# Kernel optimization log

Measured on AMD Instinct MI355X. Metric: run time of the kernel, lower is better.

Reference implementation:

```python
import jax, jax.numpy as jnp
import numpy as np

VOCAB, EMB, LAYERS, OUT, N = 32000, 43, 64, 15, 524288

def setup_inputs() -> dict:
    key = jax.random.key(0)
    ks = jax.random.split(key, 8)
    emb = jax.random.normal(ks[0], (VOCAB, EMB), jnp.float32) * 0.1
    emb = emb.at[0].set(0.0)  # padding_idx=0
    return {
        "tokens": jax.random.randint(ks[1], (N,), 0, VOCAB, jnp.int32),
        "emb": emb,
        "w_ih": jax.random.normal(ks[2], (LAYERS, 4 * EMB, EMB), jnp.float32) * 0.1,
        "w_hh": jax.random.normal(ks[3], (LAYERS, 4 * EMB, EMB), jnp.float32) * 0.1,
        "b_ih": jax.random.normal(ks[4], (LAYERS, 4 * EMB), jnp.float32) * 0.1,
        "b_hh": jax.random.normal(ks[5], (LAYERS, 4 * EMB), jnp.float32) * 0.1,
        "w_out": jax.random.normal(ks[6], (OUT, EMB), jnp.float32) * 0.1,
        "b_out": jax.random.normal(ks[7], (OUT,), jnp.float32) * 0.1,
    }

def reference(tokens, emb, w_ih, w_hh, b_ih, b_hh, w_out, b_out):
    # embedding lookup; dropout is identity in eval mode
    x = emb[tokens]  # (N, EMB)

    # 64-layer LSTM stack, seq_len=1, h0=c0=0 => f-gate * c_prev and W_hh @ h_prev vanish,
    # but we implement the full PyTorch LSTM cell math (gate order i, f, g, o).
    def layer(h, params):
        wi, wh, bi, bh = params
        h_prev = jnp.zeros_like(h)  # initial hidden state per layer
        gates = h @ wi.T + bi + h_prev @ wh.T + bh  # (N, 4*EMB)
        i, f, g, o = jnp.split(gates, 4, axis=-1)
        c = jax.nn.sigmoid(f) * 0.0 + jax.nn.sigmoid(i) * jnp.tanh(g)
        h_new = jax.nn.sigmoid(o) * jnp.tanh(c)
        return h_new, None

    h, _ = jax.lax.scan(layer, x, (w_ih, w_hh, b_ih, b_hh))
    logits = h @ w_out.T + b_out  # (N, OUT)
    return jax.nn.log_softmax(logits, axis=1)
```

## Files before the change

### kernel.cpp

```cpp
#include <hip/hip_runtime.h>

#define LAYERS 64
#define EMBD   43
#define NOUT   15
#define NTOK   524288

#define ROWB     128
#define WROWS    144
#define IMGBYTES (WROWS * ROWB)
#define NCHUNK   18

#define MBLK    256
#define THREADS 256

#define NEG_L2E   -1.44269504f
#define NEG_2L2E  -2.88539008f

typedef short bf16x8 __attribute__((ext_vector_type(8)));
typedef float f32x4  __attribute__((ext_vector_type(4)));
typedef float f32x2  __attribute__((ext_vector_type(2)));

__device__ __forceinline__ unsigned short f2bf(float f) {
  unsigned int u = __builtin_bit_cast(unsigned int, f);
  u = u + 0x7fffu + ((u >> 16) & 1u);
  return (unsigned short)(u >> 16);
}
__device__ __forceinline__ float bf2f(unsigned short s) {
  unsigned int u = ((unsigned int)s) << 16;
  return __builtin_bit_cast(float, u);
}

__global__ void pack_w_kernel(const float* __restrict__ w_ih,
                              const float* __restrict__ b_ih,
                              const float* __restrict__ b_hh,
                              unsigned char* __restrict__ wpack) {
  int idx = blockIdx.x * blockDim.x + threadIdx.x;
  if (idx >= LAYERS * WROWS) return;
  int l = idx / WROWS, n = idx % WROWS;
  int t = n >> 4, c = n & 15;
  int G = t / 3, gidx = t % 3;
  int gsel = (gidx == 0) ? 0 : ((gidx == 1) ? 2 : 3);
  float scale = (gidx == 1) ? NEG_2L2E : NEG_L2E;
  int j = (G == 0) ? 2 * c : ((G == 1) ? 2 * c + 1 : 32 + c);
  int valid = (j < EMBD);
  const float* src = w_ih + ((size_t)l * 172 + (size_t)gsel * EMBD + j) * EMBD;
  float bias = 0.0f;
  if (valid) {
    int R = gsel * EMBD + j;
    bias = (b_ih[l * 172 + R] + b_hh[l * 172 + R]) * scale;
  }
  unsigned char* dst = wpack + (size_t)l * IMGBYTES + n * ROWB;
  #pragma unroll
  for (int g = 0; g < 8; ++g) {
    union { unsigned short s[8]; uint4 v; } pk;
    #pragma unroll
    for (int e = 0; e < 8; ++e) {
      int k = g * 8 + e;
      unsigned short val = 0;
      if (valid && k < EMBD) val = f2bf(src[k] * scale);
      else if (valid && k == EMBD) val = f2bf(bias);
      pk.s[e] = val;
    }
    int slot = g ^ (n & 7);
    *(uint4*)(dst + slot * 16) = pk.v;
  }
}

__global__ void __launch_bounds__(THREADS, 3) lstm_kernel(
    const int* __restrict__ tokens,
    const float* __restrict__ emb,
    const unsigned char* __restrict__ wpack,
    const float* __restrict__ w_out,
    const float* __restrict__ b_out,
    float* __restrict__ out) {
  __shared__ __align__(16) unsigned char Hs[MBLK * ROWB];
  __shared__ __align__(16) unsigned char Ws[IMGBYTES];

  const int tid  = threadIdx.x;
  const int lane = tid & 63;
  const int wave = tid >> 6;
  const int c    = lane & 15;
  const int q    = lane >> 4;
  const int row_base = blockIdx.x * MBLK;

  {
    const unsigned char* src = wpack;
    #pragma unroll
    for (int ch = 0; ch < 5; ++ch) {
      int chunk = wave + ch * 4;
      if (chunk < NCHUNK)
        __builtin_amdgcn_global_load_lds(
            (const __attribute__((address_space(1))) void*)(src + chunk * 1024 + lane * 16),
            (__attribute__((address_space(3))) void*)(Ws + chunk * 1024),
            16, 0, 0);
    }
  }

  {
    int r = tid;
    int tok = tokens[row_base + r];
    const float* e = emb + (size_t)tok * EMBD;
    unsigned short v[64];
    #pragma unroll
    for (int k = 0; k < EMBD; ++k) v[k] = f2bf(e[k]);
    v[EMBD] = 0x3F80;
    #pragma unroll
    for (int k = EMBD + 1; k < 64; ++k) v[k] = 0;
    #pragma unroll
    for (int g = 0; g < 8; ++g) {
      union { unsigned short s[8]; uint4 u; } pk;
      #pragma unroll
      for (int e2 = 0; e2 < 8; ++e2) pk.s[e2] = v[g * 8 + e2];
      *(uint4*)(Hs + r * ROWB + ((g ^ (r & 7)) * 16)) = pk.u;
    }
  }

  int adrA0, adrA1, adrB0, adrB1, adrP[4], adrS[4];
  {
    int ra = wave * 64 + c;
    adrA0 = ra * ROWB + ((q ^ (c & 7)) * 16);
    adrA1 = ra * ROWB + (((4 + q) ^ (c & 7)) * 16);
    adrB0 = c * ROWB + ((q ^ (c & 7)) * 16);
    adrB1 = c * ROWB + (((4 + q) ^ (c & 7)) * 16);
    #pragma unroll
    for (int r4 = 0; r4 < 4; ++r4) {
      int rq = q * 4 + r4;
      int rm = rq & 7;
      int rr = wave * 64 + rq;
      adrP[r4] = rr * ROWB + (((c >> 2) ^ rm) * 16) + (c & 3) * 4;
      adrS[r4] = rr * ROWB + (((4 + (c >> 3)) ^ rm) * 16) + (c & 7) * 2;
    }
  }
  __syncthreads();

  const f32x4 zf = {0.0f, 0.0f, 0.0f, 0.0f};

  #pragma unroll 1
  for (int l = 0; l < LAYERS; ++l) {
    bf16x8 A0[4], A1[4];
    #pragma unroll
    for (int st = 0; st < 4; ++st) {
      A0[st] = *(const bf16x8*)(Hs + adrA0 + st * 2048);
      A1[st] = *(const bf16x8*)(Hs + adrA1 + st * 2048);
    }

    float hh[16];

    #pragma unroll
    for (int G = 0; G < 3; ++G) {
      f32x4 acc[3][4];
      #pragma unroll
      for (int t2 = 0; t2 < 3; ++t2) {
        int off = (G * 3 + t2) * 2048;
        bf16x8 B0 = *(const bf16x8*)(Ws + adrB0 + off);
        #pragma unroll
        for (int st = 0; st < 4; ++st)
          acc[t2][st] = __builtin_amdgcn_mfma_f32_16x16x32_bf16(A0[st], B0, zf, 0, 0, 0);
      }
      #pragma unroll
      for (int t2 = 0; t2 < 3; ++t2) {
        int off = (G * 3 + t2) * 2048;
        bf16x8 B1 = *(const bf16x8*)(Ws + adrB1 + off);
        #pragma unroll
        for (int st = 0; st < 4; ++st)
          acc[t2][st] = __builtin_amdgcn_mfma_f32_16x16x32_bf16(A1[st], B1, acc[t2][st], 0, 0, 0);
      }

      if (G == 2) {
        __syncthreads();
        if (l + 1 < LAYERS) {
          const unsigned char* src = wpack + (size_t)(l + 1) * IMGBYTES;
          #pragma unroll
          for (int ch = 0; ch < 5; ++ch) {
            int chunk = wave + ch * 4;
            if (chunk < NCHUNK)
              __builtin_amdgcn_global_load_lds(
                  (const __attribute__((address_space(1))) void*)(src + chunk * 1024 + lane * 16),
                  (__attribute__((address_space(3))) void*)(Ws + chunk * 1024),
                  16, 0, 0);
          }
        }
      }

      #pragma unroll
      for (int st = 0; st < 4; ++st) {
        #pragma unroll
        for (int hp = 0; hp < 2; ++hp) {
          const int r0 = hp * 2, r1 = hp * 2 + 1;
          f32x2 t1, t2v, t3;
          t1[0]  = __builtin_amdgcn_exp2f(acc[0][st][r0]);
          t1[1]  = __builtin_amdgcn_exp2f(acc[0][st][r1]);
          t2v[0] = __builtin_amdgcn_exp2f(acc[1][st][r0]);
          t2v[1] = __builtin_amdgcn_exp2f(acc[1][st][r1]);
          t3[0]  = __builtin_amdgcn_exp2f(acc[2][st][r0]);
          t3[1]  = __builtin_amdgcn_exp2f(acc[2][st][r1]);
          const f32x2 one = {1.0f, 1.0f};
          const f32x2 two = {2.0f, 2.0f};
          const f32x2 k15 = {15.0f, 15.0f};
          const f32x2 k25 = {2.5f, 2.5f};
          const f32x2 k6  = {6.0f, 6.0f};
          f32x2 u   = t2v + one;
          f32x2 Qd  = __builtin_elementwise_fma(t1, u, u);
          f32x2 P   = two - u;
          f32x2 x   = P * P;
          f32x2 y   = Qd * Qd;
          f32x2 n1  = __builtin_elementwise_fma(y, k15, x);
          f32x2 dt  = __builtin_elementwise_fma(y, k25, x);
          f32x2 nP  = P * n1;
          f32x2 dQ  = Qd * dt;
          f32x2 v6  = __builtin_elementwise_fma(t3, k6, k6);
          f32x2 den = dQ * v6;
          float h0 = nP[0] * __builtin_amdgcn_rcpf(den[0]);
          float h1 = nP[1] * __builtin_amdgcn_rcpf(den[1]);
          if (G == 0) {
            hh[st * 4 + r0] = h0;
            hh[st * 4 + r1] = h1;
          } else if (G == 1) {
            {
              unsigned int u0 = __builtin_bit_cast(unsigned int, hh[st * 4 + r0]) + 0x8000u;
              unsigned int u1 = __builtin_bit_cast(unsigned int, h0) + 0x8000u;
              unsigned int pk = __builtin_amdgcn_perm(u1, u0, 0x07060302u);
              *(unsigned int*)(Hs + adrP[r0] + st * 2048) = pk;
            }
            {
              unsigned int u0 = __builtin_bit_cast(unsigned int, hh[st * 4 + r1]) + 0x8000u;
              unsigned int u1 = __builtin_bit_cast(unsigned int, h1) + 0x8000u;
              unsigned int pk = __builtin_amdgcn_perm(u1, u0, 0x07060302u);
              *(unsigned int*)(Hs + adrP[r1] + st * 2048) = pk;
            }
          } else if (c <= 10) {
            unsigned int u1 = (__builtin_bit_cast(unsigned int, h0) + 0x8000u) >> 16;
            *(unsigned short*)(Hs + adrS[r0] + st * 2048) = (unsigned short)u1;
            unsigned int u2 = (__builtin_bit_cast(unsigned int, h1) + 0x8000u) >> 16;
            *(unsigned short*)(Hs + adrS[r1] + st * 2048) = (unsigned short)u2;
          }
        }
      }
    }
    __syncthreads();
  }

  {
    int r = tid;
    float h[EMBD];
    #pragma unroll
    for (int g = 0; g < 6; ++g) {
      union { uint4 u; unsigned short s[8]; } pk;
      pk.u = *(const uint4*)(Hs + r * ROWB + ((g ^ (r & 7)) * 16));
      #pragma unroll
      for (int e2 = 0; e2 < 8; ++e2) {
        int k = g * 8 + e2;
        if (k < EMBD) h[k] = bf2f(pk.s[e2]);
      }
    }
    float logit[NOUT];
    #pragma unroll
    for (int o = 0; o < NOUT; ++o) {
      float sum = b_out[o];
      #pragma unroll
      for (int k = 0; k < EMBD; ++k) sum += w_out[o * EMBD + k] * h[k];
      logit[o] = sum;
    }
    float m = logit[0];
    #pragma unroll
    for (int o = 1; o < NOUT; ++o) m = fmaxf(m, logit[o]);
    float ss = 0.0f;
    #pragma unroll
    for (int o = 0; o < NOUT; ++o) ss += __expf(logit[o] - m);
    float lse = m + __logf(ss);
    float* dst = out + (size_t)(row_base + r) * NOUT;
    #pragma unroll
    for (int o = 0; o < NOUT; ++o) dst[o] = logit[o] - lse;
  }
}

extern "C" void kernel_launch(void* const* d_in, const int* in_sizes, int n_in,
                              void* d_out, int out_size, void* d_ws, size_t ws_size,
                              hipStream_t stream) {
  const int* tokens     = (const int*)d_in[0];
  const float* emb      = (const float*)d_in[1];
  const float* w_ih     = (const float*)d_in[2];
  const float* b_ih     = (const float*)d_in[4];
  const float* b_hh     = (const float*)d_in[5];
  const float* w_out    = (const float*)d_in[6];
  const float* b_out    = (const float*)d_in[7];
  float* out            = (float*)d_out;

  const size_t need = (size_t)LAYERS * IMGBYTES;
  unsigned char* wpack = (ws_size >= need) ? (unsigned char*)d_ws
                                           : (unsigned char*)d_in[3];

  pack_w_kernel<<<(LAYERS * WROWS + 255) / 256, 256, 0, stream>>>(w_ih, b_ih, b_hh, wpack);
  lstm_kernel<<<NTOK / MBLK, THREADS, 0, stream>>>(tokens, emb, wpack, w_out, b_out, out);
}
```

Baseline: 1.058 ms.

## Shrink LDS row stride to 96 bytes to fit four blocks per CU

Cuts the padded K dimension from 64 to 48 bf16 per row for both the hidden-state tile and the weight image, using a new swizzle for the shorter rows. Lanes in the upper half of the second K step read from a small zeroed LDS region instead of real data. Total LDS per block drops from about 50KB to about 38KB, and launch bounds are raised from 3 to 4 blocks per CU to get more occupancy. In exchange the addressing is more complex, bank conflicts may rise, and there is more register pressure under the tighter bound.

Measured after the change: 1.082 ms. 1.02x slower.

```diff
diff --git a/kernel.cpp b/kernel.cpp
--- a/kernel.cpp
+++ b/kernel.cpp
@@ -5,13 +5,18 @@
 #define NOUT   15
 #define NTOK   524288
 
-#define ROWB     128
-#define WROWS    144
-#define IMGBYTES (WROWS * ROWB)
-#define NCHUNK   18
-
 #define MBLK    256
 #define THREADS 256
+
+#define ROWB      96
+#define WROWS     144
+#define IMGBYTES  (WROWS * ROWB)
+#define IMGSTRIDE 14336
+#define NCHUNK    14
+
+#define HSBYTES   (MBLK * ROWB)
+#define ZOFF      (HSBYTES + IMGSTRIDE)
+#define SBYTES    (ZOFF + 16)
 
 #define NEG_L2E   -1.44269504f
 #define NEG_2L2E  -2.88539008f
@@ -28,6 +33,11 @@
 __device__ __forceinline__ float bf2f(unsigned short s) {
   unsigned int u = ((unsigned int)s) << 16;
   return __builtin_bit_cast(float, u);
+}
+
+__device__ __forceinline__ int slotbyte(int g, int row) {
+  return (g < 4) ? (((g + (row >> 2)) & 3) * 16)
+                 : (64 + (((g - 4) ^ ((row >> 2) & 1)) * 16));
 }
 
 __global__ void pack_w_kernel(const float* __restrict__ w_ih,
@@ -49,9 +59,9 @@
     int R = gsel * EMBD + j;
     bias = (b_ih[l * 172 + R] + b_hh[l * 172 + R]) * scale;
   }
-  unsigned char* dst = wpack + (size_t)l * IMGBYTES + n * ROWB;
+  unsigned char* dst = wpack + (size_t)l * IMGSTRIDE + n * ROWB;
   #pragma unroll
-  for (int g = 0; g < 8; ++g) {
+  for (int g = 0; g < 6; ++g) {
     union { unsigned short s[8]; uint4 v; } pk;
     #pragma unroll
     for (int e = 0; e < 8; ++e) {
@@ -61,20 +71,18 @@
       else if (valid && k == EMBD) val = f2bf(bias);
       pk.s[e] = val;
     }
-    int slot = g ^ (n & 7);
-    *(uint4*)(dst + slot * 16) = pk.v;
-  }
-}
-
-__global__ void __launch_bounds__(THREADS, 3) lstm_kernel(
+    *(uint4*)(dst + slotbyte(g, n)) = pk.v;
+  }
+}
+
+__global__ void __launch_bounds__(THREADS, 4) lstm_kernel(
     const int* __restrict__ tokens,
     const float* __restrict__ emb,
     const unsigned char* __restrict__ wpack,
     const float* __restrict__ w_out,
     const float* __restrict__ b_out,
     float* __restrict__ out) {
-  __shared__ __align__(16) unsigned char Hs[MBLK * ROWB];
-  __shared__ __align__(16) unsigned char Ws[IMGBYTES];
+  __shared__ __align__(16) unsigned char S[SBYTES];
 
   const int tid  = threadIdx.x;
   const int lane = tid & 63;
@@ -86,12 +94,12 @@
   {
     const unsigned char* src = wpack;
     #pragma unroll
-    for (int ch = 0; ch < 5; ++ch) {
+    for (int ch = 0; ch < 4; ++ch) {
       int chunk = wave + ch * 4;
       if (chunk < NCHUNK)
         __builtin_amdgcn_global_load_lds(
             (const __attribute__((address_space(1))) void*)(src + chunk * 1024 + lane * 16),
-            (__attribute__((address_space(3))) void*)(Ws + chunk * 1024),
+            (__attribute__((address_space(3))) void*)(S + HSBYTES + chunk * 1024),
             16, 0, 0);
     }
   }
@@ -100,35 +108,44 @@
     int r = tid;
     int tok = tokens[row_base + r];
     const float* e = emb + (size_t)tok * EMBD;
-    unsigned short v[64];
+    unsigned short v[48];
     #pragma unroll
     for (int k = 0; k < EMBD; ++k) v[k] = f2bf(e[k]);
     v[EMBD] = 0x3F80;
     #pragma unroll
-    for (int k = EMBD + 1; k < 64; ++k) v[k] = 0;
-    #pragma unroll
-    for (int g = 0; g < 8; ++g) {
+    for (int k = EMBD + 1; k < 48; ++k) v[k] = 0;
+    #pragma unroll
+    for (int g = 0; g < 6; ++g) {
       union { unsigned short s[8]; uint4 u; } pk;
       #pragma unroll
       for (int e2 = 0; e2 < 8; ++e2) pk.s[e2] = v[g * 8 + e2];
-      *(uint4*)(Hs + r * ROWB + ((g ^ (r & 7)) * 16)) = pk.u;
-    }
-  }
-
-  int adrA0, adrA1, adrB0, adrB1, adrP[4], adrS[4];
+      *(uint4*)(S + r * ROWB + slotbyte(g, r)) = pk.u;
+    }
+    if (tid == 0) {
+      uint4 z4 = {0u, 0u, 0u, 0u};
+      *(uint4*)(S + ZOFF) = z4;
+    }
+  }
+
+  int adrA0, adrA1, adrB0, adrB1, incHi, adrP[4], adrSg[4];
   {
     int ra = wave * 64 + c;
-    adrA0 = ra * ROWB + ((q ^ (c & 7)) * 16);
-    adrA1 = ra * ROWB + (((4 + q) ^ (c & 7)) * 16);
-    adrB0 = c * ROWB + ((q ^ (c & 7)) * 16);
-    adrB1 = c * ROWB + (((4 + q) ^ (c & 7)) * 16);
+    adrA0 = ra * ROWB + (((q + (c >> 2)) & 3) * 16);
+    adrB0 = HSBYTES + c * ROWB + (((q + (c >> 2)) & 3) * 16);
+    if (q < 2) {
+      adrA1 = ra * ROWB + 64 + ((q ^ ((c >> 2) & 1)) * 16);
+      adrB1 = HSBYTES + c * ROWB + 64 + ((q ^ ((c >> 2) & 1)) * 16);
+      incHi = 16 * ROWB;
+    } else {
+      adrA1 = ZOFF;
+      adrB1 = ZOFF;
+      incHi = 0;
+    }
     #pragma unroll
     for (int r4 = 0; r4 < 4; ++r4) {
-      int rq = q * 4 + r4;
-      int rm = rq & 7;
-      int rr = wave * 64 + rq;
-      adrP[r4] = rr * ROWB + (((c >> 2) ^ rm) * 16) + (c & 3) * 4;
-      adrS[r4] = rr * ROWB + (((4 + (c >> 3)) ^ rm) * 16) + (c & 7) * 2;
+      int rr = wave * 64 + q * 4 + r4;
+      adrP[r4]  = rr * ROWB + ((((c >> 2) + q) & 3) * 16) + (c & 3) * 4;
+      adrSg[r4] = rr * ROWB + 64 + (((c >> 3) ^ (q & 1)) * 16) + (c & 7) * 2;
     }
   }
   __syncthreads();
@@ -138,29 +155,34 @@
   #pragma unroll 1
   for (int l = 0; l < LAYERS; ++l) {
     bf16x8 A0[4], A1[4];
-    #pragma unroll
-    for (int st = 0; st < 4; ++st) {
-      A0[st] = *(const bf16x8*)(Hs + adrA0 + st * 2048);
-      A1[st] = *(const bf16x8*)(Hs + adrA1 + st * 2048);
+    {
+      int a1 = adrA1;
+      #pragma unroll
+      for (int st = 0; st < 4; ++st) {
+        A0[st] = *(const bf16x8*)(S + adrA0 + st * (16 * ROWB));
+        A1[st] = *(const bf16x8*)(S + a1);
+        a1 += incHi;
+      }
     }
 
     float hh[16];
+    int b1 = adrB1;
 
     #pragma unroll
     for (int G = 0; G < 3; ++G) {
       f32x4 acc[3][4];
       #pragma unroll
       for (int t2 = 0; t2 < 3; ++t2) {
-        int off = (G * 3 + t2) * 2048;
-        bf16x8 B0 = *(const bf16x8*)(Ws + adrB0 + off);
+        int off = (G * 3 + t2) * (16 * ROWB);
+        bf16x8 B0 = *(const bf16x8*)(S + adrB0 + off);
         #pragma unroll
         for (int st = 0; st < 4; ++st)
           acc[t2][st] = __builtin_amdgcn_mfma_f32_16x16x32_bf16(A0[st], B0, zf, 0, 0, 0);
       }
       #pragma unroll
       for (int t2 = 0; t2 < 3; ++t2) {
-        int off = (G * 3 + t2) * 2048;
-        bf16x8 B1 = *(const bf16x8*)(Ws + adrB1 + off);
+        bf16x8 B1 = *(const bf16x8*)(S + b1);
+        b1 += incHi;
         #pragma unroll
         for (int st = 0; st < 4; ++st)
           acc[t2][st] = __builtin_amdgcn_mfma_f32_16x16x32_bf16(A1[st], B1, acc[t2][st], 0, 0, 0);
@@ -169,14 +191,14 @@
       if (G == 2) {
         __syncthreads();
         if (l + 1 < LAYERS) {
-          const unsigned char* src = wpack + (size_t)(l + 1) * IMGBYTES;
+          const unsigned char* src = wpack + (size_t)(l + 1) * IMGSTRIDE;
           #pragma unroll
-          for (int ch = 0; ch < 5; ++ch) {
+          for (int ch = 0; ch < 4; ++ch) {
             int chunk = wave + ch * 4;
             if (chunk < NCHUNK)
               __builtin_amdgcn_global_load_lds(
                   (const __attribute__((address_space(1))) void*)(src + chunk * 1024 + lane * 16),
-                  (__attribute__((address_space(3))) void*)(Ws + chunk * 1024),
+                  (__attribute__((address_space(3))) void*)(S + HSBYTES + chunk * 1024),
                   16, 0, 0);
           }
         }
@@ -220,19 +242,19 @@
               unsigned int u0 = __builtin_bit_cast(unsigned int, hh[st * 4 + r0]) + 0x8000u;
               unsigned int u1 = __builtin_bit_cast(unsigned int, h0) + 0x8000u;
               unsigned int pk = __builtin_amdgcn_perm(u1, u0, 0x07060302u);
-              *(unsigned int*)(Hs + adrP[r0] + st * 2048) = pk;
+              *(unsigned int*)(S + adrP[r0] + st * (16 * ROWB)) = pk;
             }
             {
               unsigned int u0 = __builtin_bit_cast(unsigned int, hh[st * 4 + r1]) + 0x8000u;
               unsigned int u1 = __builtin_bit_cast(unsigned int, h1) + 0x8000u;
               unsigned int pk = __builtin_amdgcn_perm(u1, u0, 0x07060302u);
-              *(unsigned int*)(Hs + adrP[r1] + st * 2048) = pk;
+              *(unsigned int*)(S + adrP[r1] + st * (16 * ROWB)) = pk;
             }
           } else if (c <= 10) {
             unsigned int u1 = (__builtin_bit_cast(unsigned int, h0) + 0x8000u) >> 16;
-            *(unsigned short*)(Hs + adrS[r0] + st * 2048) = (unsigned short)u1;
+            *(unsigned short*)(S + adrSg[r0] + st * (16 * ROWB)) = (unsigned short)u1;
             unsigned int u2 = (__builtin_bit_cast(unsigned int, h1) + 0x8000u) >> 16;
-            *(unsigned short*)(Hs + adrS[r1] + st * 2048) = (unsigned short)u2;
+            *(unsigned short*)(S + adrSg[r1] + st * (16 * ROWB)) = (unsigned short)u2;
           }
         }
       }
@@ -246,7 +268,7 @@
     #pragma unroll
     for (int g = 0; g < 6; ++g) {
       union { uint4 u; unsigned short s[8]; } pk;
-      pk.u = *(const uint4*)(Hs + r * ROWB + ((g ^ (r & 7)) * 16));
+      pk.u = *(const uint4*)(S + r * ROWB + slotbyte(g, r));
       #pragma unroll
       for (int e2 = 0; e2 < 8; ++e2) {
         int k = g * 8 + e2;
@@ -286,7 +308,7 @@
   const float* b_out    = (const float*)d_in[7];
   float* out            = (float*)d_out;
 
-  const size_t need = (size_t)LAYERS * IMGBYTES;
+  const size_t need = (size_t)LAYERS * IMGSTRIDE;
   unsigned char* wpack = (ws_size >= need) ? (unsigned char*)d_ws
                                            : (unsigned char*)d_in[3];
 
```

## Load per-lane packed LSTM weight fragments from global, dropping LDS staging and block barriers

Applied to the files above, without the earlier changes.

The weight packer now writes each layer in an MFMA B-fragment order, so every lane can fetch its bf16x8 fragment directly from global memory with coalesced 16-byte loads. This removes the shared-memory weight image, the per-layer async global-to-LDS copies and both per-layer __syncthreads. It relies on each wave reading and writing only its own hidden-state rows. The smaller LDS footprint allows launch bounds to go from 3 to 4 blocks per CU. The cost is that weight fetches now sit on the critical path of each layer, depending on L1/L2 hit latency instead of prefetched LDS.

New measurement: 1.065 ms. About the same (+0.6%).

```diff
diff --git a/kernel.cpp b/kernel.cpp
--- a/kernel.cpp
+++ b/kernel.cpp
@@ -5,13 +5,13 @@
 #define NOUT   15
 #define NTOK   524288
 
-#define ROWB     128
-#define WROWS    144
-#define IMGBYTES (WROWS * ROWB)
-#define NCHUNK   18
-
 #define MBLK    256
 #define THREADS 256
+
+#define ROWB     128
+#define HSBYTES  (MBLK * ROWB)
+
+#define IMGSTRIDE 18432
 
 #define NEG_L2E   -1.44269504f
 #define NEG_2L2E  -2.88539008f
@@ -35,9 +35,11 @@
                               const float* __restrict__ b_hh,
                               unsigned char* __restrict__ wpack) {
   int idx = blockIdx.x * blockDim.x + threadIdx.x;
-  if (idx >= LAYERS * WROWS) return;
-  int l = idx / WROWS, n = idx % WROWS;
-  int t = n >> 4, c = n & 15;
+  if (idx >= LAYERS * 9 * 64) return;
+  int lane = idx & 63;
+  int t    = (idx >> 6) % 9;
+  int l    = idx / (9 * 64);
+  int c = lane & 15, q = lane >> 4;
   int G = t / 3, gidx = t % 3;
   int gsel = (gidx == 0) ? 0 : ((gidx == 1) ? 2 : 3);
   float scale = (gidx == 1) ? NEG_2L2E : NEG_L2E;
@@ -49,32 +51,30 @@
     int R = gsel * EMBD + j;
     bias = (b_ih[l * 172 + R] + b_hh[l * 172 + R]) * scale;
   }
-  unsigned char* dst = wpack + (size_t)l * IMGBYTES + n * ROWB;
+  unsigned char* img = wpack + (size_t)l * IMGSTRIDE + t * 2048 + lane * 16;
   #pragma unroll
-  for (int g = 0; g < 8; ++g) {
-    union { unsigned short s[8]; uint4 v; } pk;
+  for (int hf = 0; hf < 2; ++hf) {
+    union { unsigned short s16[8]; uint4 u; } pk;
     #pragma unroll
     for (int e = 0; e < 8; ++e) {
-      int k = g * 8 + e;
+      int k = hf * 32 + q * 8 + e;
       unsigned short val = 0;
       if (valid && k < EMBD) val = f2bf(src[k] * scale);
       else if (valid && k == EMBD) val = f2bf(bias);
-      pk.s[e] = val;
-    }
-    int slot = g ^ (n & 7);
-    *(uint4*)(dst + slot * 16) = pk.v;
-  }
-}
-
-__global__ void __launch_bounds__(THREADS, 3) lstm_kernel(
+      pk.s16[e] = val;
+    }
+    *(uint4*)(img + hf * 1024) = pk.u;
+  }
+}
+
+__global__ void __launch_bounds__(THREADS, 4) lstm_kernel(
     const int* __restrict__ tokens,
     const float* __restrict__ emb,
     const unsigned char* __restrict__ wpack,
     const float* __restrict__ w_out,
     const float* __restrict__ b_out,
     float* __restrict__ out) {
-  __shared__ __align__(16) unsigned char Hs[MBLK * ROWB];
-  __shared__ __align__(16) unsigned char Ws[IMGBYTES];
+  __shared__ __align__(16) unsigned char Hs[HSBYTES];
 
   const int tid  = threadIdx.x;
   const int lane = tid & 63;
@@ -84,19 +84,6 @@
   const int row_base = blockIdx.x * MBLK;
 
   {
-    const unsigned char* src = wpack;
-    #pragma unroll
-    for (int ch = 0; ch < 5; ++ch) {
-      int chunk = wave + ch * 4;
-      if (chunk < NCHUNK)
-        __builtin_amdgcn_global_load_lds(
-            (const __attribute__((address_space(1))) void*)(src + chunk * 1024 + lane * 16),
-            (__attribute__((address_space(3))) void*)(Ws + chunk * 1024),
-            16, 0, 0);
-    }
-  }
-
-  {
     int r = tid;
     int tok = tokens[row_base + r];
     const float* e = emb + (size_t)tok * EMBD;
@@ -115,13 +102,11 @@
     }
   }
 
-  int adrA0, adrA1, adrB0, adrB1, adrP[4], adrS[4];
+  int adrA0, adrA1, adrP[4], adrS[4];
   {
     int ra = wave * 64 + c;
     adrA0 = ra * ROWB + ((q ^ (c & 7)) * 16);
     adrA1 = ra * ROWB + (((4 + q) ^ (c & 7)) * 16);
-    adrB0 = c * ROWB + ((q ^ (c & 7)) * 16);
-    adrB1 = c * ROWB + (((4 + q) ^ (c & 7)) * 16);
     #pragma unroll
     for (int r4 = 0; r4 < 4; ++r4) {
       int rq = q * 4 + r4;
@@ -131,8 +116,8 @@
       adrS[r4] = rr * ROWB + (((4 + (c >> 3)) ^ rm) * 16) + (c & 7) * 2;
     }
   }
-  __syncthreads();
-
+
+  const unsigned char* wl = wpack + lane * 16;
   const f32x4 zf = {0.0f, 0.0f, 0.0f, 0.0f};
 
   #pragma unroll 1
@@ -151,35 +136,17 @@
       f32x4 acc[3][4];
       #pragma unroll
       for (int t2 = 0; t2 < 3; ++t2) {
-        int off = (G * 3 + t2) * 2048;
-        bf16x8 B0 = *(const bf16x8*)(Ws + adrB0 + off);
+        bf16x8 B0 = *(const bf16x8*)(wl + (G * 3 + t2) * 2048);
         #pragma unroll
         for (int st = 0; st < 4; ++st)
           acc[t2][st] = __builtin_amdgcn_mfma_f32_16x16x32_bf16(A0[st], B0, zf, 0, 0, 0);
       }
       #pragma unroll
       for (int t2 = 0; t2 < 3; ++t2) {
-        int off = (G * 3 + t2) * 2048;
-        bf16x8 B1 = *(const bf16x8*)(Ws + adrB1 + off);
+        bf16x8 B1 = *(const bf16x8*)(wl + (G * 3 + t2) * 2048 + 1024);
         #pragma unroll
         for (int st = 0; st < 4; ++st)
           acc[t2][st] = __builtin_amdgcn_mfma_f32_16x16x32_bf16(A1[st], B1, acc[t2][st], 0, 0, 0);
-      }
-
-      if (G == 2) {
-        __syncthreads();
-        if (l + 1 < LAYERS) {
-          const unsigned char* src = wpack + (size_t)(l + 1) * IMGBYTES;
-          #pragma unroll
-          for (int ch = 0; ch < 5; ++ch) {
-            int chunk = wave + ch * 4;
-            if (chunk < NCHUNK)
-              __builtin_amdgcn_global_load_lds(
-                  (const __attribute__((address_space(1))) void*)(src + chunk * 1024 + lane * 16),
-                  (__attribute__((address_space(3))) void*)(Ws + chunk * 1024),
-                  16, 0, 0);
-          }
-        }
       }
 
       #pragma unroll
@@ -237,7 +204,7 @@
         }
       }
     }
-    __syncthreads();
+    wl += IMGSTRIDE;
   }
 
   {
@@ -286,10 +253,10 @@
   const float* b_out    = (const float*)d_in[7];
   float* out            = (float*)d_out;
 
-  const size_t need = (size_t)LAYERS * IMGBYTES;
+  const size_t need = (size_t)LAYERS * IMGSTRIDE;
   unsigned char* wpack = (ws_size >= need) ? (unsigned char*)d_ws
                                            : (unsigned char*)d_in[3];
 
-  pack_w_kernel<<<(LAYERS * WROWS + 255) / 256, 256, 0, stream>>>(w_ih, b_ih, b_hh, wpack);
+  pack_w_kernel<<<(LAYERS * 9 * 64 + 255) / 256, 256, 0, stream>>>(w_ih, b_ih, b_hh, wpack);
   lstm_kernel<<<NTOK / MBLK, THREADS, 0, stream>>>(tokens, emb, wpack, w_out, b_out, out);
 }
```
